# Optimization experiments

Hardware: AMD Instinct MI355X
Metric: run time of the kernel (lower is better)

## Reference

```python
import jax, jax.numpy as jnp
import numpy as np

SCORE_THR = 0.5
RADII = jnp.array([0.5, 0.6, 0.7], dtype=jnp.float32)  # radius_dict[c]; all labels 0..C-1 covered

B, N, C = 2, 8192, 3


def setup_inputs() -> dict:
    key = jax.random.key(0)
    k1, k2 = jax.random.split(key)
    xyz = jax.random.normal(k1, (B, N, 3), dtype=jnp.float32)
    cls_features = jax.random.normal(k2, (B, N, C), dtype=jnp.float32)
    return {"xyz": xyz, "cls_features": cls_features}


def _greedy_select(xyz, cls_features):
    """Greedy per-class radius suppression over the flattened batch.
    Returns sample_idx (B, L) int32, zero-padded exactly like the torch code
    (sample_idx is zeros except slot i of the batch owning selection i)."""
    b, n, _ = xyz.shape
    L = b * n
    scores = jax.nn.sigmoid(jnp.max(cls_features, axis=2))   # (B, N)
    labels = jnp.argmax(cls_features, axis=2)                # (B, N)
    valid = scores >= SCORE_THR

    flat_scores = jnp.where(valid, scores, -jnp.inf).reshape(L)
    order = jnp.argsort(-flat_scores)                        # descending score; invalid sink to end
    sorted_labels = labels.reshape(L)[order]
    sorted_valid = valid.reshape(L)[order]
    sorted_batch = (order // n).astype(jnp.int32)
    sorted_pts = xyz.reshape(L, 3)[order]

    def cond(state):
        i, remaining, _ = state
        return remaining.any() & (i < L)

    def body(state):
        i, remaining, sel_pos = state
        cur = jnp.argmax(remaining)                  # first remaining point in sorted order
        # NB: faithful to the original bug: radius chosen via sorted_labels[i]
        # (loop counter), not the label of the current point.
        r = RADII[sorted_labels[i]]
        d2 = jnp.sum((sorted_pts - sorted_pts[cur]) ** 2, axis=-1)  # (L,)
        suppress = (sorted_batch == sorted_batch[cur]) & (d2 <= r * r)
        return (i + 1, remaining & ~suppress, sel_pos.at[i].set(cur.astype(jnp.int32)))

    sel0 = jnp.full((L,), -1, dtype=jnp.int32)
    _, _, sel_pos = jax.lax.while_loop(cond, body, (jnp.int32(0), sorted_valid, sel0))

    picked = sel_pos >= 0
    orig = jnp.where(picked, order[jnp.maximum(sel_pos, 0)], 0)  # flat index in [0, L)
    bidx = jnp.where(picked, orig // n, 0)
    pidx = jnp.where(picked, orig % n, 0)
    slots = jnp.arange(L)
    # zeros init + scatter exactly mirrors torch: sample_idx[batch, i] = point
    sample_idx = jnp.zeros((b, L), dtype=jnp.int32).at[bidx, slots].set(pidx.astype(jnp.int32))
    return sample_idx


def reference(xyz, cls_features):
    sample_idx = _greedy_select(xyz, cls_features)
    bsz = xyz.shape[0]
    # gather_operation: new_xyz[b, m] = xyz[b, sample_idx[b, m]]
    new_xyz = xyz[jnp.arange(bsz)[:, None], sample_idx]          # (B, L, 3)
    return new_xyz, sample_idx
```

## Files before the change

kernel.cpp:

```cpp
#include <hip/hip_runtime.h>
#include <stdint.h>


#define L_TOT 16384
#define NPT   8192

__device__ __forceinline__ int cellco(float v) {
    int c = (int)floorf((v + 6.4f) * 1.25f);
    return c < 0 ? 0 : (c > 15 ? 15 : c);
}

__global__ void k0_init(uint16_t* __restrict__ sample, int* __restrict__ cellcnt,
                        int* __restrict__ vcount) {
    int t = blockIdx.x * blockDim.x + threadIdx.x;
    if (t < 16384) ((int*)sample)[t] = 0;
    if (t < 8192) cellcnt[t] = 0;
    if (t == 0) vcount[0] = 0;
}

__global__ void k1_keys(const float* __restrict__ cls, uint64_t* __restrict__ keys,
                        uint8_t* __restrict__ umeta, int* __restrict__ vcount) {
    int l = blockIdx.x * blockDim.x + threadIdx.x;
    if (l >= L_TOT) return;
    float c0 = cls[l * 3 + 0], c1 = cls[l * 3 + 1], c2 = cls[l * 3 + 2];
    float m = c0; int lab = 0;
    if (c1 > m) { m = c1; lab = 1; }
    if (c2 > m) { m = c2; lab = 2; }
    int valid = (m >= 0.0f) ? 1 : 0;
    float keyf = valid ? m : -__builtin_inff();
    uint32_t u = __float_as_uint(keyf);
    uint32_t o = (u & 0x80000000u) ? ~u : (u | 0x80000000u);
    keys[l] = ((uint64_t)(~o) << 32) | (uint32_t)l;
    umeta[l] = (uint8_t)(lab | (valid << 2));
    if (valid) atomicAdd(vcount, 1);
}

__global__ void __launch_bounds__(256) k2_sort(
    const uint64_t* __restrict__ keys, const uint8_t* __restrict__ umeta,
    const float* __restrict__ xyz,
    float4* __restrict__ spts, uint8_t* __restrict__ slab, uint16_t* __restrict__ sorder,
    int* __restrict__ cellcnt) {
    __shared__ uint64_t tile[2048];
    __shared__ int psum[256];
    const int t = threadIdx.x;
    const int elem = t & 31, part = t >> 5;
    const int l = blockIdx.x * 32 + elem;
    const uint64_t myk = keys[l];
    int cnt = 0;
    for (int t0 = 0; t0 < L_TOT; t0 += 2048) {
        for (int j = t; j < 2048; j += 256) tile[j] = keys[t0 + j];
        __syncthreads();
        const int b0 = part * 256;
        #pragma unroll 4
        for (int j = 0; j < 256; ++j) cnt += (tile[b0 + j] < myk) ? 1 : 0;
        __syncthreads();
    }
    psum[t] = cnt;
    __syncthreads();
    if (t < 32) {
        int rank = 0;
        #pragma unroll
        for (int q = 0; q < 8; ++q) rank += psum[q * 32 + t];
        const int ll = blockIdx.x * 32 + t;
        int b = ll >> 13, p = ll & (NPT - 1);
        const float* src = xyz + ((size_t)(b * NPT + p)) * 3;
        float x = src[0], y = src[1], z = src[2];
        uint8_t mt = umeta[ll];
        int lab = mt & 3, valid = (mt >> 2) & 1;
        float4 v; v.x = x; v.y = y; v.z = z;
        v.w = __uint_as_float((uint32_t)(b | (valid << 1)));
        spts[rank] = v;
        slab[rank] = (uint8_t)lab;
        sorder[rank] = (uint16_t)ll;
        if (valid) {
            int cl = (b << 12) | (cellco(z) << 8) | (cellco(y) << 4) | cellco(x);
            atomicAdd(&cellcnt[cl], 1);
        }
    }
}

__global__ void g2_scan(int* __restrict__ cellcnt, int* __restrict__ cellstart) {
    __shared__ int part[256];
    __shared__ int poff[256];
    int t = threadIdx.x;
    int base = t * 32;
    int loc[32];
    int s = 0;
    for (int k = 0; k < 32; ++k) { loc[k] = cellcnt[base + k]; s += loc[k]; }
    part[t] = s;
    __syncthreads();
    if (t == 0) {
        int run = 0;
        for (int q = 0; q < 256; ++q) { poff[q] = run; run += part[q]; }
    }
    __syncthreads();
    int run = poff[t];
    for (int k = 0; k < 32; ++k) {
        cellstart[base + k] = run; run += loc[k];
        cellcnt[base + k] = 0;
    }
    if (t == 255) cellstart[8192] = run;
}

__global__ void g3_scatter(const float4* __restrict__ spts, const int* __restrict__ cellstart,
                           int* __restrict__ cellfill, float4* __restrict__ cellxyz) {
    int pos = blockIdx.x * blockDim.x + threadIdx.x;
    if (pos >= L_TOT) return;
    float4 v = spts[pos];
    uint32_t w = __float_as_uint(v.w);
    if (!(w & 2u)) return;
    int b = (int)(w & 1u);
    int cl = (b << 12) | (cellco(v.z) << 8) | (cellco(v.y) << 4) | cellco(v.x);
    int slot = atomicAdd(&cellfill[cl], 1);
    float4 o; o.x = v.x; o.y = v.y; o.z = v.z; o.w = __uint_as_float((uint32_t)pos);
    cellxyz[cellstart[cl] + slot] = o;
}

__global__ void __launch_bounds__(1024) k3_greedy(
    const float4* __restrict__ spts, const uint8_t* __restrict__ slab,
    const uint16_t* __restrict__ sorder,
    const int* __restrict__ cellstart, const float4* __restrict__ cellxyz,
    const int* __restrict__ vcount, uint16_t* __restrict__ sample) {
    __shared__ uint32_t rem[512];
    __shared__ uint16_t cs16[8193];
    __shared__ float4   pkd[2][64];
    __shared__ int      pkb[2][64];
    __shared__ int      pkn[2];
    __shared__ int      win_pos[64];
    __shared__ int      s_done;

    const int t = threadIdx.x;
    const int V = vcount[0];
    for (int j = t; j < 8193; j += 1024) cs16[j] = (uint16_t)cellstart[j];
    for (int w = t; w < 512; w += 1024) {
        int lo = w * 32;
        uint32_t m;
        if (V >= lo + 32) m = 0xFFFFFFFFu;
        else if (V <= lo) m = 0u;
        else m = (1u << (V - lo)) - 1u;
        rem[w] = m;
    }
    if (t < 2) pkn[t] = 0;
    if (t == 0) s_done = 0;
    __syncthreads();

    int ii = 0;
    for (int phase = 0; phase < 32768; ++phase) {
        const int cur = phase & 1, nx = cur ^ 1;
        if (t < 64) {
            uint32_t wv[8];
            int cnt = 0;
            #pragma unroll
            for (int q = 0; q < 8; ++q) {
                wv[q] = ((volatile uint32_t*)rem)[t * 8 + q];
                cnt += __popc(wv[q]);
            }
            int pre = cnt;
            #pragma unroll
            for (int off = 1; off < 64; off <<= 1) {
                int nb = __shfl_up(pre, off);
                if (t >= off) pre += nb;
            }
            const int total = __shfl(pre, 63);
            if (total == 0) {
                if (t == 0) { s_done = 1; pkn[nx] = 0; }
            } else {
                int r = pre - cnt;
                if (r < 64) {
                    #pragma unroll
                    for (int q = 0; q < 8; ++q) {
                        if (r >= 64) break;
                        uint32_t m = wv[q];
                        while (m && r < 64) {
                            int b = __builtin_ctz(m);
                            m &= m - 1;
                            win_pos[r] = (t * 8 + q) * 32 + b;
                            ++r;
                        }
                    }
                }
                __builtin_amdgcn_wave_barrier();
                asm volatile("s_waitcnt lgkmcnt(0)" ::: "memory");
                __builtin_amdgcn_wave_barrier();
                const int nwin = total < 64 ? total : 64;
                const bool inw = (t < nwin);
                float4 v = make_float4(1e30f, 1e30f, 1e30f, 0.0f);
                int ord = 0;
                if (inw) {
                    int pos = win_pos[t];
                    v = spts[pos];
                    ord = (int)sorder[pos];
                }
                const int myb = (int)(__float_as_uint(v.w) & 1u);
                int oi = ii + t;
                int lb = slab[oi < L_TOT ? oi : (L_TOT - 1)];
                float rr = (lb == 0) ? 0.5f : ((lb == 1) ? 0.6f : 0.7f);
                float r2s = __fmul_rn(rr, rr);
                bool alive = inw;
                const int npp = pkn[cur];
                for (int j = 0; j < npp; ++j) {
                    float4 pk = pkd[cur][j];
                    if (pkb[cur][j] == myb) {
                        float dx = __fsub_rn(v.x, pk.x);
                        float dy = __fsub_rn(v.y, pk.y);
                        float dz = __fsub_rn(v.z, pk.z);
                        float d2 = __fadd_rn(__fadd_rn(__fmul_rn(dx, dx), __fmul_rn(dy, dy)),
                                             __fmul_rn(dz, dz));
                        if (d2 <= pk.w) alive = false;
                    }
                }
                unsigned long long am = __ballot(alive ? 1 : 0);
                int np = 0;
                while (am) {
                    int jp = (int)__builtin_ctzll(am);
                    float px = __shfl(v.x, jp);
                    float py = __shfl(v.y, jp);
                    float pz = __shfl(v.z, jp);
                    int   pb = __shfl(myb, jp);
                    float r2 = __shfl(r2s, np);
                    if (t == jp) {
                        pkd[nx][np] = make_float4(v.x, v.y, v.z, r2);
                        pkb[nx][np] = myb;
                        sample[myb * L_TOT + ii + np] = (uint16_t)(ord & (NPT - 1));
                    }
                    if (alive && t > jp && myb == pb) {
                        float dx = __fsub_rn(v.x, px);
                        float dy = __fsub_rn(v.y, py);
                        float dz = __fsub_rn(v.z, pz);
                        float d2 = __fadd_rn(__fadd_rn(__fmul_rn(dx, dx), __fmul_rn(dy, dy)),
                                             __fmul_rn(dz, dz));
                        if (d2 <= r2) alive = false;
                    }
                    ++np;
                    unsigned long long bal = __ballot(alive ? 1 : 0);
                    am = (jp >= 63) ? 0ull : (bal & (~0ull << (jp + 1)));
                }
                ii += np;
                if (t == 0) pkn[nx] = np;
            }
        } else {
            const int np = pkn[cur];
            if (np > 0) {
                const int tid = t - 64;
                const int ntask = np * 216;
                for (int task = tid; task < ntask; task += 960) {
                    int sub = task & 7;
                    int pc = task >> 3;
                    int p = pc / 27;
                    int c = pc - p * 27;
                    float4 pv = pkd[cur][p];
                    int pb_ = pkb[cur][p];
                    float r2 = pv.w;
                    int cx = cellco(pv.x) + (c % 3) - 1;
                    int cy = cellco(pv.y) + ((c / 3) % 3) - 1;
                    int cz = cellco(pv.z) + (c / 9) - 1;
                    if ((unsigned)cx > 15u || (unsigned)cy > 15u || (unsigned)cz > 15u) continue;
                    float lox = -6.4f + 0.8f * cx, hix = lox + 0.8f;
                    float loy = -6.4f + 0.8f * cy, hiy = loy + 0.8f;
                    float loz = -6.4f + 0.8f * cz, hiz = loz + 0.8f;
                    if (cx == 0) lox = -1e30f;  if (cx == 15) hix = 1e30f;
                    if (cy == 0) loy = -1e30f;  if (cy == 15) hiy = 1e30f;
                    if (cz == 0) loz = -1e30f;  if (cz == 15) hiz = 1e30f;
                    float dx = fmaxf(fmaxf(lox - pv.x, pv.x - hix), 0.0f);
                    float dy = fmaxf(fmaxf(loy - pv.y, pv.y - hiy), 0.0f);
                    float dz = fmaxf(fmaxf(loz - pv.z, pv.z - hiz), 0.0f);
                    if (dx * dx + dy * dy + dz * dz > r2 + 0.02f) continue;
                    int cl = (pb_ << 12) | (cz << 8) | (cy << 4) | cx;
                    int st = (int)cs16[cl];
                    int en = (int)cs16[cl + 1];
                    for (int k = st + sub; k < en; k += 8) {
                        float4 q = cellxyz[k];
                        float ddx = __fsub_rn(q.x, pv.x);
                        float ddy = __fsub_rn(q.y, pv.y);
                        float ddz = __fsub_rn(q.z, pv.z);
                        float d2 = __fadd_rn(__fadd_rn(__fmul_rn(ddx, ddx), __fmul_rn(ddy, ddy)),
                                             __fmul_rn(ddz, ddz));
                        if (d2 <= r2) {
                            uint32_t qp = __float_as_uint(q.w);
                            atomicAnd(&rem[qp >> 5], ~(1u << (qp & 31)));
                        }
                    }
                }
            }
        }
        __syncthreads();
        if (s_done) break;
    }
}

__global__ void k4_out(const float* __restrict__ xyz, const uint16_t* __restrict__ sample,
                       float* __restrict__ out) {
    int s = blockIdx.x * blockDim.x + threadIdx.x;
    if (s >= 2 * L_TOT) return;
    int idx = (int)sample[s];
    int b = s >> 14;
    const float* src = xyz + ((size_t)(b * NPT + idx)) * 3;
    float* dst = out + (size_t)s * 3;
    dst[0] = src[0]; dst[1] = src[1]; dst[2] = src[2];
    out[3 * 2 * L_TOT + s] = (float)idx;
}

extern "C" void kernel_launch(void* const* d_in, const int* in_sizes, int n_in,
                              void* d_out, int out_size, void* d_ws, size_t ws_size,
                              hipStream_t stream) {
    const float* xyz = (const float*)d_in[0];
    const float* cls = (const float*)d_in[1];
    float* out = (float*)d_out;
    char* ws = (char*)d_ws;
    float4*   spts    = (float4*)  (ws + 0);
    uint8_t*  slab    = (uint8_t*) (ws + 262144);
    uint16_t* sorder  = (uint16_t*)(ws + 278528);
    int*      cellcnt = (int*)     (ws + 311296);
    int*      cellst  = (int*)     (ws + 344064);
    float4*   cellxyz = (float4*)  (ws + 380928);
    uint64_t* keys    = (uint64_t*)(ws + 380928);
    uint8_t*  umeta   = (uint8_t*) (ws + 512000);
    uint16_t* sample  = (uint16_t*)(ws + 643072);
    int*      vcount  = (int*)     (ws + 708608);

    k0_init   <<<128, 256, 0, stream>>>(sample, cellcnt, vcount);
    k1_keys   <<<64,  256, 0, stream>>>(cls, keys, umeta, vcount);
    k2_sort   <<<512, 256, 0, stream>>>(keys, umeta, xyz, spts, slab, sorder, cellcnt);
    g2_scan   <<<1,   256, 0, stream>>>(cellcnt, cellst);
    g3_scatter<<<64,  256, 0, stream>>>(spts, cellst, cellcnt, cellxyz);
    k3_greedy <<<1,  1024, 0, stream>>>(spts, slab, sorder, cellst, cellxyz, vcount, sample);
    k4_out    <<<128, 256, 0, stream>>>(xyz, sample, out);
}
```

Measured before the change: 597.5 us.

## Pipeline greedy selection with 128-wide windows and a four-deep pick ring

The greedy kernel's leader wave now evaluates 128 candidates per phase, two per lane, and checks them against picks from the previous two phases. Grid suppression by the other waves lags one phase behind, and gathered candidates are cleared from the remaining mask up front. This is meant to overlap the serial leader-wave selection with the parallel cell-grid suppression and to halve the number of block-wide barrier phases. Separately, the init kernel is folded into the key kernel and the valid count is read from the cell prefix sum instead of an atomic. The price is more per-candidate checks against pending picks, plus the complexity of keeping the ring bookkeeping correct.

Measured after the change: 630.8 us. 1.06x slower.

```diff
diff --git a/kernel.cpp b/kernel.cpp
--- a/kernel.cpp
+++ b/kernel.cpp
@@ -9,19 +9,19 @@
     int c = (int)floorf((v + 6.4f) * 1.25f);
     return c < 0 ? 0 : (c > 15 ? 15 : c);
 }
-
-__global__ void k0_init(uint16_t* __restrict__ sample, int* __restrict__ cellcnt,
-                        int* __restrict__ vcount) {
-    int t = blockIdx.x * blockDim.x + threadIdx.x;
-    if (t < 16384) ((int*)sample)[t] = 0;
-    if (t < 8192) cellcnt[t] = 0;
-    if (t == 0) vcount[0] = 0;
+__device__ __forceinline__ float d2f(float ax, float ay, float az,
+                                     float bx, float by, float bz) {
+    float dx = __fsub_rn(ax, bx), dy = __fsub_rn(ay, by), dz = __fsub_rn(az, bz);
+    return __fadd_rn(__fadd_rn(__fmul_rn(dx, dx), __fmul_rn(dy, dy)), __fmul_rn(dz, dz));
 }
 
 __global__ void k1_keys(const float* __restrict__ cls, uint64_t* __restrict__ keys,
-                        uint8_t* __restrict__ umeta, int* __restrict__ vcount) {
+                        uint8_t* __restrict__ umeta, uint16_t* __restrict__ sample,
+                        int* __restrict__ cellcnt) {
     int l = blockIdx.x * blockDim.x + threadIdx.x;
     if (l >= L_TOT) return;
+    ((uint32_t*)sample)[l] = 0;
+    if (l < 8192) cellcnt[l] = 0;
     float c0 = cls[l * 3 + 0], c1 = cls[l * 3 + 1], c2 = cls[l * 3 + 2];
     float m = c0; int lab = 0;
     if (c1 > m) { m = c1; lab = 1; }
@@ -32,7 +32,6 @@
     uint32_t o = (u & 0x80000000u) ? ~u : (u | 0x80000000u);
     keys[l] = ((uint64_t)(~o) << 32) | (uint32_t)l;
     umeta[l] = (uint8_t)(lab | (valid << 2));
-    if (valid) atomicAdd(vcount, 1);
 }
 
 __global__ void __launch_bounds__(256) k2_sort(
@@ -120,17 +119,17 @@
     const float4* __restrict__ spts, const uint8_t* __restrict__ slab,
     const uint16_t* __restrict__ sorder,
     const int* __restrict__ cellstart, const float4* __restrict__ cellxyz,
-    const int* __restrict__ vcount, uint16_t* __restrict__ sample) {
+    uint16_t* __restrict__ sample) {
     __shared__ uint32_t rem[512];
     __shared__ uint16_t cs16[8193];
-    __shared__ float4   pkd[2][64];
-    __shared__ int      pkb[2][64];
-    __shared__ int      pkn[2];
-    __shared__ int      win_pos[64];
+    __shared__ float4   pkd[4][128];
+    __shared__ int      pkb[4][128];
+    __shared__ int      pkn[4];
+    __shared__ int      win_pos[128];
     __shared__ int      s_done;
 
     const int t = threadIdx.x;
-    const int V = vcount[0];
+    const int V = cellstart[8192];
     for (int j = t; j < 8193; j += 1024) cs16[j] = (uint16_t)cellstart[j];
     for (int w = t; w < 512; w += 1024) {
         int lo = w * 32;
@@ -140,106 +139,124 @@
         else m = (1u << (V - lo)) - 1u;
         rem[w] = m;
     }
-    if (t < 2) pkn[t] = 0;
+    if (t < 4) pkn[t] = 0;
     if (t == 0) s_done = 0;
     __syncthreads();
 
-    int ii = 0;
-    for (int phase = 0; phase < 32768; ++phase) {
-        const int cur = phase & 1, nx = cur ^ 1;
-        if (t < 64) {
-            uint32_t wv[8];
-            int cnt = 0;
+    float4 cv0 = make_float4(0,0,0,0), cv1 = make_float4(0,0,0,0);
+    int cord0 = 0, cord1 = 0, cb0 = 0, cb1 = 0;
+    float cr0 = 0.f, cr1 = 0.f;
+    int ii = 0, nwin = 0;
+
+    auto gather = [&]() {
+        uint32_t wv[8]; int cnt = 0;
+        #pragma unroll
+        for (int q = 0; q < 8; ++q) {
+            wv[q] = ((volatile uint32_t*)rem)[t * 8 + q];
+            cnt += __popc(wv[q]);
+        }
+        int pre = cnt;
+        #pragma unroll
+        for (int off = 1; off < 64; off <<= 1) {
+            int nb = __shfl_up(pre, off);
+            if (t >= off) pre += nb;
+        }
+        const int total = __shfl(pre, 63);
+        if (total == 0) { if (t == 0) s_done = 1; nwin = 0; return; }
+        int r = pre - cnt;
+        uint32_t clr[8];
+        #pragma unroll
+        for (int q = 0; q < 8; ++q) clr[q] = 0u;
+        if (r < 128) {
             #pragma unroll
             for (int q = 0; q < 8; ++q) {
-                wv[q] = ((volatile uint32_t*)rem)[t * 8 + q];
-                cnt += __popc(wv[q]);
+                if (r >= 128) break;
+                uint32_t m = wv[q];
+                while (m && r < 128) {
+                    uint32_t bit = m & (~m + 1u);
+                    int b = __builtin_ctz(m);
+                    m &= m - 1u;
+                    win_pos[r] = (t * 8 + q) * 32 + b;
+                    clr[q] |= bit;
+                    ++r;
+                }
             }
-            int pre = cnt;
-            #pragma unroll
-            for (int off = 1; off < 64; off <<= 1) {
-                int nb = __shfl_up(pre, off);
-                if (t >= off) pre += nb;
-            }
-            const int total = __shfl(pre, 63);
-            if (total == 0) {
-                if (t == 0) { s_done = 1; pkn[nx] = 0; }
-            } else {
-                int r = pre - cnt;
-                if (r < 64) {
-                    #pragma unroll
-                    for (int q = 0; q < 8; ++q) {
-                        if (r >= 64) break;
-                        uint32_t m = wv[q];
-                        while (m && r < 64) {
-                            int b = __builtin_ctz(m);
-                            m &= m - 1;
-                            win_pos[r] = (t * 8 + q) * 32 + b;
-                            ++r;
-                        }
+        }
+        #pragma unroll
+        for (int q = 0; q < 8; ++q)
+            if (clr[q]) atomicAnd(&rem[t * 8 + q], ~clr[q]);
+        for (int z = total + t; z < 128; z += 64) win_pos[z] = 0;
+        __builtin_amdgcn_wave_barrier();
+        asm volatile("s_waitcnt lgkmcnt(0)" ::: "memory");
+        __builtin_amdgcn_wave_barrier();
+        nwin = total < 128 ? total : 128;
+        int p0 = win_pos[t], p1 = win_pos[64 + t];
+        cv0 = spts[p0]; cv1 = spts[p1];
+        cord0 = (int)sorder[p0]; cord1 = (int)sorder[p1];
+        cb0 = cord0 >> 13; cb1 = cord1 >> 13;
+        int o0 = ii + t;       o0 = o0 > (L_TOT - 1) ? (L_TOT - 1) : o0;
+        int o1 = ii + 64 + t;  o1 = o1 > (L_TOT - 1) ? (L_TOT - 1) : o1;
+        int l0 = slab[o0], l1 = slab[o1];
+        float rr0 = (l0 == 0) ? 0.5f : ((l0 == 1) ? 0.6f : 0.7f);
+        float rr1 = (l1 == 0) ? 0.5f : ((l1 == 1) ? 0.6f : 0.7f);
+        cr0 = __fmul_rn(rr0, rr0); cr1 = __fmul_rn(rr1, rr1);
+    };
+
+    if (t < 64) gather();
+    __syncthreads();
+
+    for (int ph = 0; ph < 4096; ++ph) {
+        const int cur = ph & 3, prev1 = (ph + 3) & 3, prev2 = (ph + 2) & 3;
+        if (t < 64) {
+            int np = 0;
+            if (nwin > 0) {
+                bool a0 = (t < nwin), a1 = (64 + t < nwin);
+                #pragma unroll 1
+                for (int rs = 0; rs < 2; ++rs) {
+                    const int ring = (rs == 0) ? prev1 : prev2;
+                    const int m = pkn[ring];
+                    for (int j = 0; j < m; ++j) {
+                        float4 pk = pkd[ring][j];
+                        int pb = pkb[ring][j];
+                        if (a0 && cb0 == pb &&
+                            d2f(cv0.x, cv0.y, cv0.z, pk.x, pk.y, pk.z) <= pk.w) a0 = false;
+                        if (a1 && cb1 == pb &&
+                            d2f(cv1.x, cv1.y, cv1.z, pk.x, pk.y, pk.z) <= pk.w) a1 = false;
                     }
                 }
-                __builtin_amdgcn_wave_barrier();
-                asm volatile("s_waitcnt lgkmcnt(0)" ::: "memory");
-                __builtin_amdgcn_wave_barrier();
-                const int nwin = total < 64 ? total : 64;
-                const bool inw = (t < nwin);
-                float4 v = make_float4(1e30f, 1e30f, 1e30f, 0.0f);
-                int ord = 0;
-                if (inw) {
-                    int pos = win_pos[t];
-                    v = spts[pos];
-                    ord = (int)sorder[pos];
-                }
-                const int myb = (int)(__float_as_uint(v.w) & 1u);
-                int oi = ii + t;
-                int lb = slab[oi < L_TOT ? oi : (L_TOT - 1)];
-                float rr = (lb == 0) ? 0.5f : ((lb == 1) ? 0.6f : 0.7f);
-                float r2s = __fmul_rn(rr, rr);
-                bool alive = inw;
-                const int npp = pkn[cur];
-                for (int j = 0; j < npp; ++j) {
-                    float4 pk = pkd[cur][j];
-                    if (pkb[cur][j] == myb) {
-                        float dx = __fsub_rn(v.x, pk.x);
-                        float dy = __fsub_rn(v.y, pk.y);
-                        float dz = __fsub_rn(v.z, pk.z);
-                        float d2 = __fadd_rn(__fadd_rn(__fmul_rn(dx, dx), __fmul_rn(dy, dy)),
-                                             __fmul_rn(dz, dz));
-                        if (d2 <= pk.w) alive = false;
+                unsigned long long am0 = __ballot(a0 ? 1 : 0);
+                unsigned long long am1 = __ballot(a1 ? 1 : 0);
+                while (am0 | am1) {
+                    const int js = am0 ? 0 : 1;
+                    const int jl = am0 ? (int)__builtin_ctzll(am0)
+                                       : (int)__builtin_ctzll(am1);
+                    float px = __shfl(js ? cv1.x : cv0.x, jl);
+                    float py = __shfl(js ? cv1.y : cv0.y, jl);
+                    float pz = __shfl(js ? cv1.z : cv0.z, jl);
+                    int   pb = __shfl(js ? cb1 : cb0, jl);
+                    float r2 = __shfl((np & 64) ? cr1 : cr0, np & 63);
+                    if (t == jl) {
+                        int    b_ = js ? cb1 : cb0;
+                        int    o_ = js ? cord1 : cord0;
+                        float  x_ = js ? cv1.x : cv0.x;
+                        float  y_ = js ? cv1.y : cv0.y;
+                        float  z_ = js ? cv1.z : cv0.z;
+                        pkd[cur][np] = make_float4(x_, y_, z_, r2);
+                        pkb[cur][np] = b_;
+                        sample[b_ * L_TOT + ii + np] = (uint16_t)(o_ & (NPT - 1));
                     }
-                }
-                unsigned long long am = __ballot(alive ? 1 : 0);
-                int np = 0;
-                while (am) {
-                    int jp = (int)__builtin_ctzll(am);
-                    float px = __shfl(v.x, jp);
-                    float py = __shfl(v.y, jp);
-                    float pz = __shfl(v.z, jp);
-                    int   pb = __shfl(myb, jp);
-                    float r2 = __shfl(r2s, np);
-                    if (t == jp) {
-                        pkd[nx][np] = make_float4(v.x, v.y, v.z, r2);
-                        pkb[nx][np] = myb;
-                        sample[myb * L_TOT + ii + np] = (uint16_t)(ord & (NPT - 1));
-                    }
-                    if (alive && t > jp && myb == pb) {
-                        float dx = __fsub_rn(v.x, px);
-                        float dy = __fsub_rn(v.y, py);
-                        float dz = __fsub_rn(v.z, pz);
-                        float d2 = __fadd_rn(__fadd_rn(__fmul_rn(dx, dx), __fmul_rn(dy, dy)),
-                                             __fmul_rn(dz, dz));
-                        if (d2 <= r2) alive = false;
-                    }
+                    if (a0 && cb0 == pb && d2f(cv0.x, cv0.y, cv0.z, px, py, pz) <= r2) a0 = false;
+                    if (a1 && cb1 == pb && d2f(cv1.x, cv1.y, cv1.z, px, py, pz) <= r2) a1 = false;
                     ++np;
-                    unsigned long long bal = __ballot(alive ? 1 : 0);
-                    am = (jp >= 63) ? 0ull : (bal & (~0ull << (jp + 1)));
+                    am0 = __ballot(a0 ? 1 : 0);
+                    am1 = __ballot(a1 ? 1 : 0);
                 }
                 ii += np;
-                if (t == 0) pkn[nx] = np;
             }
+            if (t == 0) pkn[cur] = np;
+            gather();
         } else {
-            const int np = pkn[cur];
+            const int np = pkn[prev1];
             if (np > 0) {
                 const int tid = t - 64;
                 const int ntask = np * 216;
@@ -248,8 +265,8 @@
                     int pc = task >> 3;
                     int p = pc / 27;
                     int c = pc - p * 27;
-                    float4 pv = pkd[cur][p];
-                    int pb_ = pkb[cur][p];
+                    float4 pv = pkd[prev1][p];
+                    int pb_ = pkb[prev1][p];
                     float r2 = pv.w;
                     int cx = cellco(pv.x) + (c % 3) - 1;
                     int cy = cellco(pv.y) + ((c / 3) % 3) - 1;
@@ -265,16 +282,11 @@
                     float dy = fmaxf(fmaxf(loy - pv.y, pv.y - hiy), 0.0f);
                     float dz = fmaxf(fmaxf(loz - pv.z, pv.z - hiz), 0.0f);
                     if (dx * dx + dy * dy + dz * dz > r2 + 0.02f) continue;
-                    int cl = (pb_ << 12) | (cz << 8) | (cy << 4) | cx;
-                    int st = (int)cs16[cl];
-                    int en = (int)cs16[cl + 1];
+                    int st = (int)cs16[(pb_ << 12) | (cz << 8) | (cy << 4) | cx];
+                    int en = (int)cs16[((pb_ << 12) | (cz << 8) | (cy << 4) | cx) + 1];
                     for (int k = st + sub; k < en; k += 8) {
                         float4 q = cellxyz[k];
-                        float ddx = __fsub_rn(q.x, pv.x);
-                        float ddy = __fsub_rn(q.y, pv.y);
-                        float ddz = __fsub_rn(q.z, pv.z);
-                        float d2 = __fadd_rn(__fadd_rn(__fmul_rn(ddx, ddx), __fmul_rn(ddy, ddy)),
-                                             __fmul_rn(ddz, ddz));
+                        float d2 = d2f(q.x, q.y, q.z, pv.x, pv.y, pv.z);
                         if (d2 <= r2) {
                             uint32_t qp = __float_as_uint(q.w);
                             atomicAnd(&rem[qp >> 5], ~(1u << (qp & 31)));
@@ -316,13 +328,11 @@
     uint64_t* keys    = (uint64_t*)(ws + 380928);
     uint8_t*  umeta   = (uint8_t*) (ws + 512000);
     uint16_t* sample  = (uint16_t*)(ws + 643072);
-    int*      vcount  = (int*)     (ws + 708608);
-
-    k0_init   <<<128, 256, 0, stream>>>(sample, cellcnt, vcount);
-    k1_keys   <<<64,  256, 0, stream>>>(cls, keys, umeta, vcount);
+
+    k1_keys   <<<64,  256, 0, stream>>>(cls, keys, umeta, sample, cellcnt);
     k2_sort   <<<512, 256, 0, stream>>>(keys, umeta, xyz, spts, slab, sorder, cellcnt);
     g2_scan   <<<1,   256, 0, stream>>>(cellcnt, cellst);
     g3_scatter<<<64,  256, 0, stream>>>(spts, cellst, cellcnt, cellxyz);
-    k3_greedy <<<1,  1024, 0, stream>>>(spts, slab, sorder, cellst, cellxyz, vcount, sample);
+    k3_greedy <<<1,  1024, 0, stream>>>(spts, slab, sorder, cellst, cellxyz, sample);
     k4_out    <<<128, 256, 0, stream>>>(xyz, sample, out);
 }
```
